# Kernel tuning notes

Hardware: AMD Instinct MI355X
Metric: run time of the kernel (lower is better)

The kernel has to match this reference:

```python
import jax, jax.numpy as jnp
import numpy as np

R = 32            # voxel resolution
ALPHA = 0.1       # LeakyReLU slope
BN_EPS = 1e-4     # BatchNormalization epsilon
VOX_EPS = 1e-6    # Voxelization eps (normalize=True)


def _bn_train(x, gamma, beta, axes):
    # training-mode batch norm over `axes`, channel axis = 1
    mean = jnp.mean(x, axes, keepdims=True)
    var = jnp.var(x, axes, keepdims=True)
    bshape = (1, -1) + (1,) * (x.ndim - 2)
    return gamma.reshape(bshape) * (x - mean) * jax.lax.rsqrt(var + BN_EPS) + beta.reshape(bshape)


def _lrelu(x):
    return jnp.where(x >= 0, x, ALPHA * x)


def _voxelize(features, coords):
    # features [B,C,N], coords [B,3,N] -> grid [B,C,R,R,R], norm_coords [B,3,N] in [0,R-1]
    centered = coords - jnp.mean(coords, axis=2, keepdims=True)
    max_norm = jnp.max(jnp.linalg.norm(centered, axis=1, keepdims=True), axis=2, keepdims=True)
    norm = centered / (max_norm * 2.0 + VOX_EPS) + 0.5
    norm = jnp.clip(norm * R, 0.0, R - 1)
    vox = jnp.round(norm).astype(jnp.int32)              # [B,3,N]
    flat = (vox[:, 0] * R + vox[:, 1]) * R + vox[:, 2]   # [B,N]

    def per_batch(f, idx):  # f [C,N], idx [N]
        sums = jax.ops.segment_sum(f.T, idx, num_segments=R ** 3)            # [R^3,C]
        cnt = jax.ops.segment_sum(jnp.ones_like(idx, f.dtype), idx, num_segments=R ** 3)
        return (sums / jnp.maximum(cnt, 1.0)[:, None]).T                      # [C,R^3]

    grid = jax.vmap(per_batch)(features, flat)            # [B,C,R^3]
    B, C = features.shape[0], features.shape[1]
    return grid.reshape(B, C, R, R, R), norm


def _conv3d(x, w, b):
    # x [B,C,D,H,W], w [k,k,k,Cin,Cout], 'same' padding
    y = jax.lax.conv_general_dilated(x, w, (1, 1, 1), 'SAME',
                                     dimension_numbers=('NCDHW', 'DHWIO', 'NCDHW'))
    return y + b.reshape(1, -1, 1, 1, 1)


def _trilinear_devoxelize(vf, coords):
    # vf [B,C,R^3], coords [B,3,N] in [0,R-1] -> [B,C,N]
    c0f = jnp.clip(jnp.floor(coords), 0.0, R - 1)
    frac = coords - c0f                                   # [B,3,N]
    c0 = c0f.astype(jnp.int32)
    c1 = jnp.minimum(c0 + 1, R - 1)
    out = jnp.zeros((vf.shape[0], vf.shape[1], coords.shape[2]), vf.dtype)
    for dx in (0, 1):
        for dy in (0, 1):
            for dz in (0, 1):
                xs = c1[:, 0] if dx else c0[:, 0]
                ys = c1[:, 1] if dy else c0[:, 1]
                zs = c1[:, 2] if dz else c0[:, 2]
                w = ((frac[:, 0] if dx else 1 - frac[:, 0]) *
                     (frac[:, 1] if dy else 1 - frac[:, 1]) *
                     (frac[:, 2] if dz else 1 - frac[:, 2]))           # [B,N]
                idx = (xs * R + ys) * R + zs                            # [B,N]
                g = jnp.take_along_axis(vf, idx[:, None, :], axis=2)    # [B,C,N]
                out = out + w[:, None, :] * g
    return out


def setup_inputs() -> dict:
    key = jax.random.key(0)
    ks = jax.random.split(key, 16)
    B, C, N, K = 8, 64, 16384, 3
    s = 0.05
    return {
        'features': jax.random.normal(ks[0], (B, C, N), jnp.float32),
        'coords': jax.random.normal(ks[1], (B, 3, N), jnp.float32),
        'conv1_w': jax.random.normal(ks[2], (K, K, K, C, C), jnp.float32) * s,
        'conv1_b': jnp.zeros((C,), jnp.float32),
        'bn1_gamma': jnp.ones((C,), jnp.float32),
        'bn1_beta': jnp.zeros((C,), jnp.float32),
        'conv2_w': jax.random.normal(ks[3], (K, K, K, C, C), jnp.float32) * s,
        'conv2_b': jnp.zeros((C,), jnp.float32),
        'bn2_gamma': jnp.ones((C,), jnp.float32),
        'bn2_beta': jnp.zeros((C,), jnp.float32),
        'pf_w': jax.random.normal(ks[4], (C, C), jnp.float32) * s,
        'pf_bias': jnp.zeros((C,), jnp.float32),
        'pf_gamma': jnp.ones((C,), jnp.float32),
        'pf_beta': jnp.zeros((C,), jnp.float32),
    }


def reference(features, coords, conv1_w, conv1_b, bn1_gamma, bn1_beta,
              conv2_w, conv2_b, bn2_gamma, bn2_beta,
              pf_w, pf_bias, pf_gamma, pf_beta):
    vgrid, norm_coords = _voxelize(features, coords)
    v = _lrelu(_bn_train(_conv3d(vgrid, conv1_w, conv1_b), bn1_gamma, bn1_beta, (0, 2, 3, 4)))
    v = _lrelu(_bn_train(_conv3d(v, conv2_w, conv2_b), bn2_gamma, bn2_beta, (0, 2, 3, 4)))
    vflat = v.reshape(v.shape[0], v.shape[1], -1)                 # [B,C,R^3]
    vpts = _trilinear_devoxelize(vflat, norm_coords)              # [B,C,N]
    # point branch: shared MLP (1x1 conv) + BN + LeakyReLU
    p = jnp.einsum('bcn,cd->bdn', features, pf_w) + pf_bias[None, :, None]
    p = _lrelu(_bn_train(p, pf_gamma, pf_beta, (0, 2)))
    return vpts + p, coords
```

## Files before the change

kernel.cpp:

```cpp
#include <hip/hip_runtime.h>
#include <stdint.h>

#define RR 32
#define R3 32768
#define NB 8
#define NCH 64
#define NP 16384

typedef unsigned short u16;
typedef uint32_t u32;
typedef __attribute__((ext_vector_type(8))) short bf8;
typedef __attribute__((ext_vector_type(4))) float f4;
typedef __attribute__((ext_vector_type(16))) float f16x;

#define MFMA(a,b,c)   __builtin_amdgcn_mfma_f32_16x16x32_bf16(a,b,c,0,0,0)
#define MFMA32(a,b,c) __builtin_amdgcn_mfma_f32_32x32x16_bf16(a,b,c,0,0,0)

__device__ __forceinline__ float bf2f(u16 v){
  union { u32 u; float f; } x; x.u = ((u32)v) << 16; return x.f;
}
__device__ __forceinline__ float u2f(u32 u){
  union { u32 u; float f; } x; x.u = u; return x.f;
}
__device__ __forceinline__ u16 f2bf(float f){
  union { float f; u32 u; } x; x.f = f;
  u32 r = x.u + 0x7fffu + ((x.u >> 16) & 1u);
  return (u16)(r >> 16);
}
__device__ __forceinline__ float ldf(const void* p, size_t i, int isbf){
  return isbf ? bf2f(((const u16*)p)[i]) : ((const float*)p)[i];
}

#define OFF_GRID  0ull
#define OFF_BUF1  33554432ull
#define OFF_FT    33554432ull
#define OFF_P     67108864ull
#define OFF_CNT   83886080ull
#define OFF_SMALL 84934656ull
#define OFF_STAT  84936704ull
#define OFF_OFFS  84948992ull
#define OFF_NC    85997568ull
#define OFF_VIDX  87570432ull
#define OFF_SORT  88094720ull
#define OFF_WF1   88619008ull
#define OFF_WF2   88840192ull
#define OFF_WFP   89061376ull
#define WS_NEED   89069568ull
#define ZOFF      OFF_CNT
#define ZBYTES    1062912ull

__global__ void k_dtype(const uint32_t* __restrict__ gamma_raw, int* __restrict__ flag){
  if (threadIdx.x == 0) *flag = (gamma_raw[0] == 0x3F800000u) ? 0 : 1;
}

__global__ __launch_bounds__(256) void k_csum(const void* __restrict__ coords, float* __restrict__ small,
                                              const int* __restrict__ dflag){
  int g = blockIdx.x;
  int b = g >> 3, chunk = g & 7;
  int tid = threadIdx.x;
  int isbf = *dflag;
  size_t cb = (size_t)b*3*NP;
  int n0 = chunk*2048;
  float sx=0.f, sy=0.f, sz=0.f;
  for (int n = n0 + tid; n < n0 + 2048; n += 256){
    sx += ldf(coords, cb+n, isbf);
    sy += ldf(coords, cb+NP+n, isbf);
    sz += ldf(coords, cb+2*NP+n, isbf);
  }
  #pragma unroll
  for (int m = 1; m <= 32; m <<= 1){
    sx += __shfl_xor(sx, m); sy += __shfl_xor(sy, m); sz += __shfl_xor(sz, m);
  }
  __shared__ float red[12];
  int wv = tid >> 6, lane = tid & 63;
  if (lane == 0){ red[wv*3+0] = sx; red[wv*3+1] = sy; red[wv*3+2] = sz; }
  __syncthreads();
  if (tid == 0){
    float tx = red[0]+red[3]+red[6]+red[9];
    float ty = red[1]+red[4]+red[7]+red[10];
    float tz = red[2]+red[5]+red[8]+red[11];
    atomicAdd(&small[384 + b*4 + 0], tx);
    atomicAdd(&small[384 + b*4 + 1], ty);
    atomicAdd(&small[384 + b*4 + 2], tz);
  }
}

__global__ __launch_bounds__(256) void k_cmax(const void* __restrict__ coords, float* __restrict__ small,
                                              const int* __restrict__ dflag){
  int g = blockIdx.x;
  int b = g >> 3, chunk = g & 7;
  int tid = threadIdx.x;
  int isbf = *dflag;
  size_t cb = (size_t)b*3*NP;
  float inv = 1.0f/NP;
  float mx = small[384+b*4+0]*inv, my = small[384+b*4+1]*inv, mz = small[384+b*4+2]*inv;
  int n0 = chunk*2048;
  float vm = 0.f;
  for (int n = n0 + tid; n < n0 + 2048; n += 256){
    float cx = ldf(coords, cb+n, isbf)      - mx;
    float cy = ldf(coords, cb+NP+n, isbf)   - my;
    float cz = ldf(coords, cb+2*NP+n, isbf) - mz;
    vm = fmaxf(vm, sqrtf(cx*cx + cy*cy + cz*cz));
  }
  #pragma unroll
  for (int m = 1; m <= 32; m <<= 1) vm = fmaxf(vm, __shfl_xor(vm, m));
  __shared__ float red[4];
  int wv = tid >> 6, lane = tid & 63;
  if (lane == 0) red[wv] = vm;
  __syncthreads();
  if (tid == 0){
    float t = fmaxf(fmaxf(red[0], red[1]), fmaxf(red[2], red[3]));
    atomicMax((unsigned*)&small[384 + b*4 + 3], __float_as_uint(t));
  }
}

__global__ void k_pointprep(const void* __restrict__ coords, const float* __restrict__ small,
                            float* __restrict__ nc, int* __restrict__ vidx, int* __restrict__ cnt,
                            void* __restrict__ out0, const int* __restrict__ dflag){
  int g = blockIdx.x*256 + threadIdx.x;
  int isbf = *dflag;
  int b = g >> 14; int n = g & (NP-1);
  float inv = 1.0f/NP;
  float mx = small[384+b*4+0]*inv, my = small[384+b*4+1]*inv, mz = small[384+b*4+2]*inv;
  float vm = small[384+b*4+3];
  float sc = 1.0f / (2.0f*vm + 1e-6f);
  size_t cb = (size_t)b*3*NP;
  size_t ob = (size_t)NB*NCH*NP + cb + n;
  if (isbf){
    const u16* cs = (const u16*)coords; u16* o = (u16*)out0;
    o[ob] = cs[cb+n]; o[ob+NP] = cs[cb+NP+n]; o[ob+2*NP] = cs[cb+2*NP+n];
  } else {
    const float* cs = (const float*)coords; float* o = (float*)out0;
    o[ob] = cs[cb+n]; o[ob+NP] = cs[cb+NP+n]; o[ob+2*NP] = cs[cb+2*NP+n];
  }
  float nx = ((ldf(coords, cb+n, isbf)      - mx)*sc + 0.5f) * 32.0f;
  float ny = ((ldf(coords, cb+NP+n, isbf)   - my)*sc + 0.5f) * 32.0f;
  float nz = ((ldf(coords, cb+2*NP+n, isbf) - mz)*sc + 0.5f) * 32.0f;
  nx = fminf(fmaxf(nx, 0.f), 31.f);
  ny = fminf(fmaxf(ny, 0.f), 31.f);
  nz = fminf(fmaxf(nz, 0.f), 31.f);
  nc[(b*3+0)*NP + n] = nx; nc[(b*3+1)*NP + n] = ny; nc[(b*3+2)*NP + n] = nz;
  int vx = (int)rintf(nx), vy = (int)rintf(ny), vz = (int)rintf(nz);
  int flat = (vx*32 + vy)*32 + vz;
  vidx[g] = flat;
  atomicAdd(&cnt[b*R3 + flat], 1);
}

__global__ __launch_bounds__(256) void k_scan1(const int* __restrict__ cnt, int* __restrict__ csum){
  int g = blockIdx.x, tid = threadIdx.x;
  const int4* c4 = (const int4*)(cnt + g*1024);
  int4 v = c4[tid];
  int s = v.x + v.y + v.z + v.w;
  #pragma unroll
  for (int m = 1; m <= 32; m <<= 1) s += __shfl_xor(s, m);
  __shared__ int red[4];
  if ((tid & 63) == 0) red[tid >> 6] = s;
  __syncthreads();
  if (tid == 0) csum[g] = red[0] + red[1] + red[2] + red[3];
}

__global__ __launch_bounds__(256) void k_scan2(int* __restrict__ csum){
  int t = threadIdx.x;
  __shared__ int part[256];
  int orig = csum[t];
  part[t] = orig; __syncthreads();
  #pragma unroll
  for (int st = 1; st <= 16; st <<= 1){
    int v = ((t & 31) >= st) ? part[t - st] : 0;
    __syncthreads();
    part[t] += v;
    __syncthreads();
  }
  csum[t] = part[t] - orig;
}

__global__ __launch_bounds__(256) void k_scan3(const int* __restrict__ cnt, const int* __restrict__ csum,
                                               int* __restrict__ off){
  int g = blockIdx.x, tid = threadIdx.x;
  int base = csum[g];
  const int4* c4 = (const int4*)(cnt + g*1024);
  int4 v = c4[tid];
  int s = v.x + v.y + v.z + v.w;
  __shared__ int part[256];
  part[tid] = s; __syncthreads();
  #pragma unroll
  for (int st = 1; st < 256; st <<= 1){
    int w = (tid >= st) ? part[tid - st] : 0;
    __syncthreads();
    part[tid] += w;
    __syncthreads();
  }
  int excl = base + part[tid] - s;
  int4 o;
  o.x = excl;
  o.y = excl + v.x;
  o.z = excl + v.x + v.y;
  o.w = excl + v.x + v.y + v.z;
  ((int4*)(off + g*1024))[tid] = o;
}

__global__ void k_sortpts(const int* __restrict__ vidx, int* __restrict__ off, int* __restrict__ sorted){
  int g = blockIdx.x*256 + threadIdx.x;
  int b = g >> 14; int n = g & (NP-1);
  int v = vidx[g];
  int slot = atomicAdd(&off[b*R3 + v], 1);
  sorted[b*NP + slot] = n;
}

__global__ __launch_bounds__(256) void k_voxsum(const u16* __restrict__ fT, const int* __restrict__ sorted,
                         const int* __restrict__ cnt, const int* __restrict__ off,
                         u16* __restrict__ grid){
  int wid = blockIdx.x*4 + (threadIdx.x >> 6);
  int lane = threadIdx.x & 63;
  int b = wid >> 11;
  int v0 = (wid & 2047) << 4;
  int base = b*R3 + v0;
  int c = 0, e = 0;
  if (lane < 16){ c = cnt[base + lane]; e = off[base + lane]; }
  int start = __shfl(e - c, 0);
  int total = __shfl(e, 15) - start;
  const int* sb = sorted + (size_t)b*NP;
  int sp = 0;
  if (lane < total) sp = sb[start + lane];
  #pragma unroll
  for (int i = 0; i < 16; i++){
    int ci = __shfl(c, i);
    int rel = __shfl(e, i) - ci - start;
    float a0 = 0.f, a1 = 0.f;
    int j = 0;
    for (; j + 1 < ci; j += 2){
      int k0 = rel + j, k1 = k0 + 1;
      int n0 = (k0 < 64) ? __shfl(sp, k0) : sb[start + k0];
      int n1 = (k1 < 64) ? __shfl(sp, k1) : sb[start + k1];
      a0 += bf2f(fT[((size_t)(b*NP + n0))*64 + lane]);
      a1 += bf2f(fT[((size_t)(b*NP + n1))*64 + lane]);
    }
    if (j < ci){
      int k0 = rel + j;
      int n0 = (k0 < 64) ? __shfl(sp, k0) : sb[start + k0];
      a0 += bf2f(fT[((size_t)(b*NP + n0))*64 + lane]);
    }
    float acc = a0 + a1;
    grid[((size_t)(base + i))*64 + lane] = f2bf(acc / (float)max(ci, 1));
  }
}

__global__ void k_wprep(const void* __restrict__ w, u16* __restrict__ wfrag, const int* __restrict__ dflag){
  int idx = blockIdx.x; int lane = threadIdx.x;
  int isbf = *dflag;
  int ntl = idx & 3; int kk = (idx >> 2) & 1; int tap = idx >> 3;
  int lh = lane & 15, quad = lane >> 4;
  int n = ntl*16 + lh;
  u16* dst = wfrag + ((size_t)idx*64 + lane)*8;
  for (int j = 0; j < 8; j++){
    int k = kk*32 + quad*8 + j;
    dst[j] = f2bf(ldf(w, (size_t)(tap*64 + k)*64 + n, isbf));
  }
}

__global__ void k_wprep32(const void* __restrict__ w, u16* __restrict__ wfrag, const int* __restrict__ dflag){
  int idx = blockIdx.x; int lane = threadIdx.x;
  int isbf = *dflag;
  int nh = idx & 1; int ks = (idx >> 1) & 3; int tap = idx >> 3;
  int n = nh*32 + (lane & 31);
  int khalf = lane >> 5;
  u16* dst = wfrag + ((size_t)idx*64 + lane)*8;
  for (int j = 0; j < 8; j++){
    int cin = ks*16 + khalf*8 + j;
    dst[j] = f2bf(ldf(w, (size_t)(tap*64 + cin)*64 + n, isbf));
  }
}

__device__ __forceinline__ void bn_params(const float* __restrict__ spread, int c, float invM,
                                          float* mean, float* rs){
  float su = 0.f, sq = 0.f;
  #pragma unroll
  for (int i = 0; i < 8; i++){ su += spread[i*128 + c]; sq += spread[i*128 + 64 + c]; }
  float m = su * invM;
  *mean = m;
  *rs = rsqrtf(sq*invM - m*m + 1e-4f);
}

#define ISSUE_W(BANK, TAP) do { \
  _Pragma("unroll") \
  for (int ks_ = 0; ks_ < 4; ks_++) \
    BANK[ks_] = *(const bf8*)(wstream + (size_t)((TAP)*4 + ks_)*1024); \
} while(0)

#define ISSUE_A8(BANK, TAP, H) do { \
  const int t_ = (TAP); \
  const int dwi_ = t_ % 3, dvi_ = (t_/3) % 3, dui_ = t_/9; \
  const u16* rp0_ = &lds_in[((2*(H) + dui_)*6 + vsel + dvi_)*2176]; \
  const u16* rp1_ = rp0_ + 6*2176; \
  const int wp_ = mlane + dwi_; \
  const int wb_ = wp_*64, wx_ = wp_ & 7; \
  _Pragma("unroll") \
  for (int ks_ = 0; ks_ < 4; ks_++){ \
    const int off_ = wb_ + ((((ks_*2) + khalf) ^ wx_) << 3); \
    BANK[ks_]     = *(const bf8*)(rp0_ + off_); \
    BANK[4 + ks_] = *(const bf8*)(rp1_ + off_); \
  } \
} while(0)

#define CONSUME(BW, BA, ACC0, ACC1) do { \
  _Pragma("unroll") \
  for (int ks_ = 0; ks_ < 4; ks_++){ \
    ACC0 = MFMA32(BA[ks_],     BW[ks_], ACC0); \
    ACC1 = MFMA32(BA[4 + ks_], BW[ks_], ACC1); \
  } \
} while(0)

template<int BN>
__global__ __launch_bounds__(512, 1) void k_conv_t(const u16* __restrict__ in, const u16* __restrict__ wfrag,
                                                   u16* __restrict__ out, const float* __restrict__ spread,
                                                   float* __restrict__ statOut,
                                                   const void* __restrict__ gamma, const void* __restrict__ beta,
                                                   const int* __restrict__ dflag){
  __shared__ u16 lds_in[36*2176];
  __shared__ float bnA[64], bnB[64];
  int bx = blockIdx.x;
  int b = bx >> 6; int r = bx & 63;
  int u0 = (r >> 3) * 4; int v0 = (r & 7) * 4;
  int tid = threadIdx.x, wv = tid >> 6, lane = tid & 63;

  if constexpr (BN){
    if (tid < 64){
      int isbf = *dflag;
      float mean, rs;
      bn_params(spread, tid, 1.0f/(NB*R3), &mean, &rs);
      float ga = ldf(gamma, tid, isbf), be = ldf(beta, tid, isbf);
      float A = ga*rs;
      bnA[tid] = A; bnB[tid] = be - mean*A;
    }
    __syncthreads();
  }

  uint4 zz; zz.x = 0; zz.y = 0; zz.z = 0; zz.w = 0;
  for (int ri = wv; ri < 36; ri += 8){
    int u2 = u0 + (ri / 6) - 1;
    int v2 = v0 + (ri % 6) - 1;
    uint4* dstrow = (uint4*)&lds_in[ri*2176];
    if ((unsigned)u2 > 31u || (unsigned)v2 > 31u){
      for (int i = lane; i < 272; i += 64) dstrow[i] = zz;
      continue;
    }
    const uint4* src = (const uint4*)(in + ((size_t)(b*R3 + (u2*32 + v2)*32))*64);
    if (lane < 8) dstrow[lane] = zz;
    else if (lane < 16) dstrow[264 + (lane & 7)] = zz;
    #pragma unroll
    for (int ch = 0; ch < 4; ch++){
      int idx = ch*64 + lane;
      int w = idx >> 3, cc = idx & 7;
      uint4 v = src[idx];
      if constexpr (BN){
        u32 in4[4] = {v.x, v.y, v.z, v.w};
        u32 o4[4];
        #pragma unroll
        for (int k = 0; k < 4; k++){
          int c = cc*8 + 2*k;
          float lo = u2f(in4[k] << 16);
          float hi = u2f(in4[k] & 0xFFFF0000u);
          lo = bnA[c]*lo + bnB[c];     lo = (lo >= 0.f) ? lo : 0.1f*lo;
          hi = bnA[c+1]*hi + bnB[c+1]; hi = (hi >= 0.f) ? hi : 0.1f*hi;
          o4[k] = (u32)f2bf(lo) | ((u32)f2bf(hi) << 16);
        }
        v.x = o4[0]; v.y = o4[1]; v.z = o4[2]; v.w = o4[3];
      }
      int wp = w + 1;
      dstrow[wp*8 + (cc ^ (wp & 7))] = v;
    }
  }
  __syncthreads();

  int vsel = wv & 3, nh = wv >> 2;
  int v_i = v0 + vsel;
  int mlane = lane & 31;
  int khalf = lane >> 5;
  f16x acc0, acc1, acc2, acc3;
  #pragma unroll
  for (int i = 0; i < 16; i++){ acc0[i] = 0.f; acc1[i] = 0.f; acc2[i] = 0.f; acc3[i] = 0.f; }

  const u16* wstream = wfrag + (size_t)nh*512 + (size_t)lane*8;

  bf8 W0[4], W1[4], W2[4];
  bf8 Aa[8], Ab[8];

  ISSUE_W(W0, 0);
  ISSUE_W(W1, 1);
  ISSUE_A8(Aa, 0, 0);

  #pragma unroll
  for (int tap = 0; tap < 27; ++tap){
    const int pf = tap + 2;
    if (pf < 27){
      if (pf % 3 == 0)      ISSUE_W(W0, pf);
      else if (pf % 3 == 1) ISSUE_W(W1, pf);
      else                  ISSUE_W(W2, pf);
    }
    ISSUE_A8(Ab, tap, 1);
    __builtin_amdgcn_sched_barrier(0);
    if (tap < 25)       asm volatile("s_waitcnt vmcnt(8) lgkmcnt(8)");
    else if (tap == 25) asm volatile("s_waitcnt vmcnt(4) lgkmcnt(8)");
    else                asm volatile("s_waitcnt vmcnt(0) lgkmcnt(8)");
    __builtin_amdgcn_sched_barrier(0);
    {
      const int wsel = tap % 3;
      if (wsel == 0)      CONSUME(W0, Aa, acc0, acc1);
      else if (wsel == 1) CONSUME(W1, Aa, acc0, acc1);
      else                CONSUME(W2, Aa, acc0, acc1);
    }
    if (tap + 1 < 27) ISSUE_A8(Aa, tap + 1, 0);
    __builtin_amdgcn_sched_barrier(0);
    if (tap < 25)       asm volatile("s_waitcnt vmcnt(8) lgkmcnt(8)");
    else if (tap == 25) asm volatile("s_waitcnt vmcnt(4) lgkmcnt(8)");
    else                asm volatile("s_waitcnt vmcnt(0) lgkmcnt(0)");
    __builtin_amdgcn_sched_barrier(0);
    {
      const int wsel = tap % 3;
      if (wsel == 0)      CONSUME(W0, Ab, acc2, acc3);
      else if (wsel == 1) CONSUME(W1, Ab, acc2, acc3);
      else                CONSUME(W2, Ab, acc2, acc3);
    }
  }

  int co = nh*32 + mlane;
  int rbase = 4*khalf;
  size_t base0 = ((size_t)(b*R3 + ((u0+0)*32 + v_i)*32))*64;
  size_t base1 = ((size_t)(b*R3 + ((u0+1)*32 + v_i)*32))*64;
  size_t base2 = ((size_t)(b*R3 + ((u0+2)*32 + v_i)*32))*64;
  size_t base3 = ((size_t)(b*R3 + ((u0+3)*32 + v_i)*32))*64;
  #pragma unroll
  for (int reg = 0; reg < 16; reg++){
    int row = (reg & 3) + 8*(reg >> 2) + rbase;
    out[base0 + (size_t)row*64 + co] = f2bf(acc0[reg]);
    out[base1 + (size_t)row*64 + co] = f2bf(acc1[reg]);
    out[base2 + (size_t)row*64 + co] = f2bf(acc2[reg]);
    out[base3 + (size_t)row*64 + co] = f2bf(acc3[reg]);
  }

  float s = 0.f, s2 = 0.f;
  #pragma unroll
  for (int reg = 0; reg < 16; reg++){
    float v0_ = acc0[reg], v1_ = acc1[reg], v2_ = acc2[reg], v3_ = acc3[reg];
    s  += v0_ + v1_ + v2_ + v3_;
    s2 += v0_*v0_ + v1_*v1_ + v2_*v2_ + v3_*v3_;
  }
  s  += __shfl_xor(s, 32);
  s2 += __shfl_xor(s2, 32);
  if (lane < 32){
    atomicAdd(&statOut[(bx & 7)*128 + co], s);
    atomicAdd(&statOut[(bx & 7)*128 + 64 + co], s2);
  }
}

__global__ __launch_bounds__(256) void k_stats2(const u16* __restrict__ buf, float* __restrict__ spread, int M){
  __shared__ float sred[4*128];
  int tid = threadIdx.x, bx = blockIdx.x;
  int wv = tid >> 6, lane = tid & 63;
  int sub = lane & 7;
  int g = bx*256 + tid;
  float s[8], s2[8];
  #pragma unroll
  for (int j = 0; j < 8; j++){ s[j] = 0.f; s2[j] = 0.f; }
  const uint4* p4 = (const uint4*)buf;
  size_t total = (size_t)M * 8;
  for (size_t f = g; f < total; f += 262144){
    uint4 v = p4[f];
    u32 ws_[4] = {v.x, v.y, v.z, v.w};
    #pragma unroll
    for (int k = 0; k < 4; k++){
      float lo = u2f(ws_[k] << 16);
      float hi = u2f(ws_[k] & 0xFFFF0000u);
      s[2*k]   += lo; s2[2*k]   += lo*lo;
      s[2*k+1] += hi; s2[2*k+1] += hi*hi;
    }
  }
  #pragma unroll
  for (int j = 0; j < 8; j++){
    #pragma unroll
    for (int m = 8; m <= 32; m <<= 1){
      s[j]  += __shfl_xor(s[j],  m);
      s2[j] += __shfl_xor(s2[j], m);
    }
  }
  if (lane < 8){
    #pragma unroll
    for (int j = 0; j < 8; j++){
      sred[wv*128 + sub*8 + j]      = s[j];
      sred[wv*128 + 64 + sub*8 + j] = s2[j];
    }
  }
  __syncthreads();
  if (tid < 128){
    float t = sred[tid] + sred[128+tid] + sred[256+tid] + sred[384+tid];
    atomicAdd(&spread[(bx & 7)*128 + tid], t);
  }
}

__global__ __launch_bounds__(256) void k_ftrans(const void* __restrict__ feat, u16* __restrict__ fT,
                                                const int* __restrict__ dflag){
  __shared__ u16 t[64*72];
  int bx = blockIdx.x;
  int isbf = *dflag;
  int b = bx >> 8; int n0 = (bx & 255) * 64;
  int tid = threadIdx.x;
  int c = tid >> 2, q = tid & 3;
  if (isbf){
    const uint4* src = (const uint4*)((const u16*)feat + ((size_t)(b*NCH + c))*NP + n0 + q*16);
    uint4 v0 = src[0], v1 = src[1];
    *(uint4*)&t[c*72 + q*16]     = v0;
    *(uint4*)&t[c*72 + q*16 + 8] = v1;
  } else {
    const float4* src = (const float4*)((const float*)feat + ((size_t)(b*NCH + c))*NP + n0 + q*16);
    #pragma unroll
    for (int h = 0; h < 4; h++){
      float4 f = src[h];
      u16* d = &t[c*72 + q*16 + h*4];
      d[0] = f2bf(f.x); d[1] = f2bf(f.y); d[2] = f2bf(f.z); d[3] = f2bf(f.w);
    }
  }
  __syncthreads();
  int n = tid >> 2, qc = tid & 3;
  union { u16 h[16]; uint4 v[2]; } pk;
  #pragma unroll
  for (int j = 0; j < 16; j++) pk.h[j] = t[(qc*16 + j)*72 + n];
  uint4* dst = (uint4*)(fT + ((size_t)(b*NP + n0 + n))*64 + qc*16);
  dst[0] = pk.v[0]; dst[1] = pk.v[1];
}

__global__ void k_pgemm(const u16* __restrict__ fT, const u16* __restrict__ wfp, u16* __restrict__ p){
  __shared__ u16 As[128*64];
  int bx = blockIdx.x;
  size_t row0 = (size_t)bx * 128;
  int tid = threadIdx.x, wv = tid >> 6, lane = tid & 63;
  const uint4* src = (const uint4*)(fT + row0*64);
  uint4* dst = (uint4*)As;
  for (int i = tid; i < 1024; i += 256) dst[i] = src[i];
  __syncthreads();
  int lh = lane & 15, quad = lane >> 4;
  f4 z4 = {0.f,0.f,0.f,0.f};
  f4 acc[2][4];
  for (int i = 0; i < 2; i++) for (int j = 0; j < 4; j++) acc[i][j] = z4;
  const u16* ap = &As[(wv*32)*64];
  #pragma unroll
  for (int kk = 0; kk < 2; kk++){
    bf8 a0 = *(const bf8*)(ap + lh*64 + kk*32 + quad*8);
    bf8 a1 = *(const bf8*)(ap + (16+lh)*64 + kk*32 + quad*8);
    #pragma unroll
    for (int ntl = 0; ntl < 4; ntl++){
      bf8 bf = *(const bf8*)(wfp + ((size_t)(kk*4 + ntl)*64 + lane)*8);
      acc[0][ntl] = MFMA(a0, bf, acc[0][ntl]);
      acc[1][ntl] = MFMA(a1, bf, acc[1][ntl]);
    }
  }
  #pragma unroll
  for (int mt = 0; mt < 2; mt++)
    for (int ntl = 0; ntl < 4; ntl++)
      for (int reg = 0; reg < 4; reg++){
        int rr = wv*32 + mt*16 + quad*4 + reg;
        p[(row0 + rr)*64 + ntl*16 + lh] = f2bf(acc[mt][ntl][reg]);
      }
}

__global__ void k_devox(const u16* __restrict__ grid, const u16* __restrict__ p,
                        const float* __restrict__ stP, const float* __restrict__ st2,
                        const void* __restrict__ pfg, const void* __restrict__ pfb,
                        const void* __restrict__ g2, const void* __restrict__ b2,
                        const float* __restrict__ nc, void* __restrict__ out0,
                        const int* __restrict__ dflag){
  __shared__ float t[64*65];
  int bx = blockIdx.x;
  int isbf = *dflag;
  int b = bx >> 8; int n0 = (bx & 255) * 64;
  int tid = threadIdx.x, wv = tid >> 6, lane = tid & 63;
  int c = lane;
  float meanP, rsP;
  bn_params(stP, c, 1.0f/(NB*NP), &meanP, &rsP);
  float gaP = ldf(pfg, c, isbf), beP = ldf(pfb, c, isbf);
  float mean2, rs2;
  bn_params(st2, c, 1.0f/(NB*R3), &mean2, &rs2);
  float ga2 = ldf(g2, c, isbf), be2 = ldf(b2, c, isbf);
  float A2 = ga2*rs2, B2 = be2 - mean2*A2;
  for (int pt = wv; pt < 64; pt += 4){
    int n = n0 + pt;
    float nx = nc[(b*3+0)*NP + n];
    float ny = nc[(b*3+1)*NP + n];
    float nz = nc[(b*3+2)*NP + n];
    float x0f = floorf(nx), y0f = floorf(ny), z0f = floorf(nz);
    int x0 = (int)x0f, y0 = (int)y0f, z0 = (int)z0f;
    float fx = nx - x0f, fy = ny - y0f, fz = nz - z0f;
    int x1 = min(x0+1,31), y1 = min(y0+1,31), z1 = min(z0+1,31);
    float acc = 0.f;
    #pragma unroll
    for (int k = 0; k < 8; k++){
      int dx = k >> 2, dy = (k >> 1) & 1, dz = k & 1;
      int xs = dx ? x1 : x0, ys = dy ? y1 : y0, zs = dz ? z1 : z0;
      float wgt = (dx ? fx : 1.f-fx)*(dy ? fy : 1.f-fy)*(dz ? fz : 1.f-fz);
      float gv = bf2f(grid[((size_t)(b*R3 + (xs*32+ys)*32 + zs))*64 + c]);
      gv = A2*gv + B2;
      gv = (gv >= 0.f) ? gv : 0.1f*gv;
      acc += wgt * gv;
    }
    float pv = bf2f(p[((size_t)(b*NP + n))*64 + c]);
    float y = gaP*(pv - meanP)*rsP + beP;
    y = (y >= 0.f) ? y : 0.1f*y;
    t[pt*65 + c] = acc + y;
  }
  __syncthreads();
  for (int cp = 0; cp < 16; cp++){
    int co = wv + cp*4;
    size_t oi = ((size_t)(b*NCH + co))*NP + n0 + lane;
    float val = t[lane*65 + co];
    if (isbf) ((u16*)out0)[oi] = f2bf(val);
    else      ((float*)out0)[oi] = val;
  }
}

extern "C" void kernel_launch(void* const* d_in, const int* in_sizes, int n_in,
                              void* d_out, int out_size, void* d_ws, size_t ws_size,
                              hipStream_t stream){
  if (ws_size < WS_NEED) return;

  const void* feat   = d_in[0];
  const void* coords = d_in[1];
  const void* w1     = d_in[2];
  const void* g1     = d_in[4];
  const void* b1     = d_in[5];
  const void* w2     = d_in[6];
  const void* g2     = d_in[8];
  const void* b2     = d_in[9];
  const void* pw     = d_in[10];
  const void* pg     = d_in[12];
  const void* pb     = d_in[13];

  char* ws = (char*)d_ws;
  u16*   gridv = (u16*)(ws + OFF_GRID);
  u16*   buf1  = (u16*)(ws + OFF_BUF1);
  u16*   fT    = (u16*)(ws + OFF_FT);
  u16*   p     = (u16*)(ws + OFF_P);
  int*   cnt   = (int*)(ws + OFF_CNT);
  float* small = (float*)(ws + OFF_SMALL);
  int*   csum  = (int*)small;
  int*   dflag = (int*)(small + 448);
  float* stat  = (float*)(ws + OFF_STAT);
  int*   offs  = (int*)(ws + OFF_OFFS);
  float* nc    = (float*)(ws + OFF_NC);
  int*   vidx  = (int*)(ws + OFF_VIDX);
  int*   sorted= (int*)(ws + OFF_SORT);
  u16*   wf1   = (u16*)(ws + OFF_WF1);
  u16*   wf2   = (u16*)(ws + OFF_WF2);
  u16*   wfp   = (u16*)(ws + OFF_WFP);

  hipMemsetAsync(ws + ZOFF, 0, ZBYTES, stream);
  k_dtype<<<1, 64, 0, stream>>>((const uint32_t*)g1, dflag);

  k_wprep32<<<27*8, 64, 0, stream>>>(w1, wf1, dflag);
  k_wprep32<<<27*8, 64, 0, stream>>>(w2, wf2, dflag);
  k_wprep<<<8, 64, 0, stream>>>(pw, wfp, dflag);

  k_csum<<<64, 256, 0, stream>>>(coords, small, dflag);
  k_cmax<<<64, 256, 0, stream>>>(coords, small, dflag);
  k_pointprep<<<NB*NP/256, 256, 0, stream>>>(coords, small, nc, vidx, cnt, d_out, dflag);
  k_scan1<<<256, 256, 0, stream>>>(cnt, csum);
  k_scan2<<<1, 256, 0, stream>>>(csum);
  k_scan3<<<256, 256, 0, stream>>>(cnt, csum, offs);
  k_sortpts<<<NB*NP/256, 256, 0, stream>>>(vidx, offs, sorted);

  k_ftrans<<<NB*NP/64, 256, 0, stream>>>(feat, fT, dflag);
  k_voxsum<<<NB*R3/64, 256, 0, stream>>>(fT, sorted, cnt, offs, gridv);
  k_pgemm<<<NB*NP/128, 256, 0, stream>>>(fT, wfp, p);
  k_stats2<<<1024, 256, 0, stream>>>(p, stat + 2048, NB*NP);

  k_conv_t<0><<<NB*64, 512, 0, stream>>>(gridv, wf1, buf1, nullptr, stat + 0, nullptr, nullptr, nullptr);
  k_conv_t<1><<<NB*64, 512, 0, stream>>>(buf1, wf2, gridv, stat + 0, stat + 1024, g1, b1, dflag);

  k_devox<<<NB*NP/64, 256, 0, stream>>>(gridv, p, stat + 2048, stat + 1024,
                                        pg, pb, g2, b2, nc, d_out, dflag);
}
```

Measured before the change: 363.2 us.

## Fuse feature transpose, point-branch GEMM and BN stats into one kernel

Merges the feature transpose, the point-branch 1x1 GEMM and the point BN statistics reduction into a single kernel. The GEMM takes its A operand directly from the shared-memory tile, and statistics are computed from the fp32 accumulators. This removes two kernel launches and the global re-reads of fT and p. In exchange, A fragments are gathered with scalar strided LDS reads, and stats are taken before bf16 rounding.

```diff
diff --git a/kernel.cpp b/kernel.cpp
--- a/kernel.cpp
+++ b/kernel.cpp
@@ -453,57 +453,16 @@
   }
 }
 
-__global__ __launch_bounds__(256) void k_stats2(const u16* __restrict__ buf, float* __restrict__ spread, int M){
-  __shared__ float sred[4*128];
-  int tid = threadIdx.x, bx = blockIdx.x;
-  int wv = tid >> 6, lane = tid & 63;
-  int sub = lane & 7;
-  int g = bx*256 + tid;
-  float s[8], s2[8];
-  #pragma unroll
-  for (int j = 0; j < 8; j++){ s[j] = 0.f; s2[j] = 0.f; }
-  const uint4* p4 = (const uint4*)buf;
-  size_t total = (size_t)M * 8;
-  for (size_t f = g; f < total; f += 262144){
-    uint4 v = p4[f];
-    u32 ws_[4] = {v.x, v.y, v.z, v.w};
-    #pragma unroll
-    for (int k = 0; k < 4; k++){
-      float lo = u2f(ws_[k] << 16);
-      float hi = u2f(ws_[k] & 0xFFFF0000u);
-      s[2*k]   += lo; s2[2*k]   += lo*lo;
-      s[2*k+1] += hi; s2[2*k+1] += hi*hi;
-    }
-  }
-  #pragma unroll
-  for (int j = 0; j < 8; j++){
-    #pragma unroll
-    for (int m = 8; m <= 32; m <<= 1){
-      s[j]  += __shfl_xor(s[j],  m);
-      s2[j] += __shfl_xor(s2[j], m);
-    }
-  }
-  if (lane < 8){
-    #pragma unroll
-    for (int j = 0; j < 8; j++){
-      sred[wv*128 + sub*8 + j]      = s[j];
-      sred[wv*128 + 64 + sub*8 + j] = s2[j];
-    }
-  }
-  __syncthreads();
-  if (tid < 128){
-    float t = sred[tid] + sred[128+tid] + sred[256+tid] + sred[384+tid];
-    atomicAdd(&spread[(bx & 7)*128 + tid], t);
-  }
-}
-
-__global__ __launch_bounds__(256) void k_ftrans(const void* __restrict__ feat, u16* __restrict__ fT,
-                                                const int* __restrict__ dflag){
+__global__ __launch_bounds__(256) void k_ftrans_pg(const void* __restrict__ feat, u16* __restrict__ fT,
+                                                   const u16* __restrict__ wfp, u16* __restrict__ p,
+                                                   float* __restrict__ statP,
+                                                   const int* __restrict__ dflag){
   __shared__ u16 t[64*72];
+  __shared__ float sred[512];
   int bx = blockIdx.x;
   int isbf = *dflag;
   int b = bx >> 8; int n0 = (bx & 255) * 64;
-  int tid = threadIdx.x;
+  int tid = threadIdx.x, wv = tid >> 6, lane = tid & 63;
   int c = tid >> 2, q = tid & 3;
   if (isbf){
     const uint4* src = (const uint4*)((const u16*)feat + ((size_t)(b*NCH + c))*NP + n0 + q*16);
@@ -520,46 +479,63 @@
     }
   }
   __syncthreads();
-  int n = tid >> 2, qc = tid & 3;
-  union { u16 h[16]; uint4 v[2]; } pk;
-  #pragma unroll
-  for (int j = 0; j < 16; j++) pk.h[j] = t[(qc*16 + j)*72 + n];
-  uint4* dst = (uint4*)(fT + ((size_t)(b*NP + n0 + n))*64 + qc*16);
-  dst[0] = pk.v[0]; dst[1] = pk.v[1];
-}
-
-__global__ void k_pgemm(const u16* __restrict__ fT, const u16* __restrict__ wfp, u16* __restrict__ p){
-  __shared__ u16 As[128*64];
-  int bx = blockIdx.x;
-  size_t row0 = (size_t)bx * 128;
-  int tid = threadIdx.x, wv = tid >> 6, lane = tid & 63;
-  const uint4* src = (const uint4*)(fT + row0*64);
-  uint4* dst = (uint4*)As;
-  for (int i = tid; i < 1024; i += 256) dst[i] = src[i];
-  __syncthreads();
+  {
+    int n = tid >> 2, qc = tid & 3;
+    union { u16 h[16]; uint4 v[2]; } pk;
+    #pragma unroll
+    for (int j = 0; j < 16; j++) pk.h[j] = t[(qc*16 + j)*72 + n];
+    uint4* dst = (uint4*)(fT + ((size_t)(b*NP + n0 + n))*64 + qc*16);
+    dst[0] = pk.v[0]; dst[1] = pk.v[1];
+  }
   int lh = lane & 15, quad = lane >> 4;
   f4 z4 = {0.f,0.f,0.f,0.f};
   f4 acc[2][4];
-  for (int i = 0; i < 2; i++) for (int j = 0; j < 4; j++) acc[i][j] = z4;
-  const u16* ap = &As[(wv*32)*64];
+  #pragma unroll
+  for (int j = 0; j < 4; j++){ acc[0][j] = z4; acc[1][j] = z4; }
+  int rowl = wv*16 + lh;
   #pragma unroll
   for (int kk = 0; kk < 2; kk++){
-    bf8 a0 = *(const bf8*)(ap + lh*64 + kk*32 + quad*8);
-    bf8 a1 = *(const bf8*)(ap + (16+lh)*64 + kk*32 + quad*8);
+    bf8 a0;
+    #pragma unroll
+    for (int j = 0; j < 8; j++) a0[j] = (short)t[(kk*32 + quad*8 + j)*72 + rowl];
     #pragma unroll
     for (int ntl = 0; ntl < 4; ntl++){
       bf8 bf = *(const bf8*)(wfp + ((size_t)(kk*4 + ntl)*64 + lane)*8);
       acc[0][ntl] = MFMA(a0, bf, acc[0][ntl]);
-      acc[1][ntl] = MFMA(a1, bf, acc[1][ntl]);
-    }
-  }
-  #pragma unroll
-  for (int mt = 0; mt < 2; mt++)
-    for (int ntl = 0; ntl < 4; ntl++)
-      for (int reg = 0; reg < 4; reg++){
-        int rr = wv*32 + mt*16 + quad*4 + reg;
-        p[(row0 + rr)*64 + ntl*16 + lh] = f2bf(acc[mt][ntl][reg]);
-      }
+    }
+  }
+  float s[4], s2[4];
+  #pragma unroll
+  for (int ntl = 0; ntl < 4; ntl++){
+    s[ntl] = 0.f; s2[ntl] = 0.f;
+    #pragma unroll
+    for (int reg = 0; reg < 4; reg++){
+      float v = acc[0][ntl][reg];
+      int rr = wv*16 + quad*4 + reg;
+      p[((size_t)(b*NP + n0 + rr))*64 + ntl*16 + lh] = f2bf(v);
+      s[ntl] += v; s2[ntl] += v*v;
+    }
+  }
+  #pragma unroll
+  for (int ntl = 0; ntl < 4; ntl++){
+    #pragma unroll
+    for (int m = 16; m <= 32; m <<= 1){
+      s[ntl]  += __shfl_xor(s[ntl],  m);
+      s2[ntl] += __shfl_xor(s2[ntl], m);
+    }
+  }
+  if (lane < 16){
+    #pragma unroll
+    for (int ntl = 0; ntl < 4; ntl++){
+      sred[wv*128 + ntl*16 + lh]      = s[ntl];
+      sred[wv*128 + 64 + ntl*16 + lh] = s2[ntl];
+    }
+  }
+  __syncthreads();
+  if (tid < 128){
+    float tot = sred[tid] + sred[128+tid] + sred[256+tid] + sred[384+tid];
+    atomicAdd(&statP[(bx & 7)*128 + tid], tot);
+  }
 }
 
 __global__ void k_devox(const u16* __restrict__ grid, const u16* __restrict__ p,
@@ -666,10 +642,8 @@
   k_scan3<<<256, 256, 0, stream>>>(cnt, csum, offs);
   k_sortpts<<<NB*NP/256, 256, 0, stream>>>(vidx, offs, sorted);
 
-  k_ftrans<<<NB*NP/64, 256, 0, stream>>>(feat, fT, dflag);
+  k_ftrans_pg<<<NB*NP/64, 256, 0, stream>>>(feat, fT, wfp, p, stat + 2048, dflag);
   k_voxsum<<<NB*R3/64, 256, 0, stream>>>(fT, sorted, cnt, offs, gridv);
-  k_pgemm<<<NB*NP/128, 256, 0, stream>>>(fT, wfp, p);
-  k_stats2<<<1024, 256, 0, stream>>>(p, stat + 2048, NB*NP);
 
   k_conv_t<0><<<NB*64, 512, 0, stream>>>(gridv, wf1, buf1, nullptr, stat + 0, nullptr, nullptr, nullptr);
   k_conv_t<1><<<NB*64, 512, 0, stream>>>(buf1, wf2, gridv, stat + 0, stat + 1024, g1, b1, dflag);
```

Result: no change. 367.8 us (+1.3%).
